# Optimization experiments

Measured on AMD Instinct MI355X. Metric: run time of the kernel, lower is better.

## Reference

```python
import jax, jax.numpy as jnp
import numpy as np

N, E = 50000, 800000
IN_DIM, HIDDEN, HEADS, EDGE_DIM, OUT_DIM = 128, 64, 4, 16, 1
NEG_SLOPE = 0.2


def gat_conv(x, src, dst, edge_attr, W, We, att_src, att_dst, att_edge, bias, heads, out_ch, concat):
    n = x.shape[0]
    h = (x @ W).reshape(n, heads, out_ch)                     # [N,H,C]
    a_src = jnp.einsum('nhc,hc->nh', h, att_src)              # [N,H]
    a_dst = jnp.einsum('nhc,hc->nh', h, att_dst)
    e = (edge_attr @ We).reshape(-1, heads, out_ch)           # [E,H,C]
    a_e = jnp.einsum('ehc,hc->eh', e, att_edge)               # [E,H]
    alpha = jax.nn.leaky_relu(a_src[src] + a_dst[dst] + a_e, NEG_SLOPE)  # [E,H]
    # per-destination-node softmax
    amax = jax.ops.segment_max(alpha, dst, num_segments=n)
    ex = jnp.exp(alpha - amax[dst])
    denom = jax.ops.segment_sum(ex, dst, num_segments=n)
    alpha = ex / (denom[dst] + 1e-16)
    msg = h[src] * alpha[..., None]                           # [E,H,C]
    out = jax.ops.segment_sum(msg, dst, num_segments=n)       # [N,H,C]
    out = out.reshape(n, heads * out_ch) if concat else out.mean(axis=1)
    return out + bias


def setup_inputs() -> dict:
    key = jax.random.key(0)
    ks = jax.random.split(key, 16)
    s = 0.1
    inp = {
        'x': jax.random.normal(ks[0], (N, IN_DIM), jnp.float32),
        'edge_index': jax.random.randint(ks[1], (2, E), 0, N, jnp.int32),
        'edge_attr': jax.random.normal(ks[2], (E, EDGE_DIM), jnp.float32),
        # layer 1: heads=4, concat=True
        'W1': jax.random.normal(ks[3], (IN_DIM, HEADS * HIDDEN), jnp.float32) * s,
        'We1': jax.random.normal(ks[4], (EDGE_DIM, HEADS * HIDDEN), jnp.float32) * s,
        'as1': jax.random.normal(ks[5], (HEADS, HIDDEN), jnp.float32) * s,
        'ad1': jax.random.normal(ks[6], (HEADS, HIDDEN), jnp.float32) * s,
        'ae1': jax.random.normal(ks[7], (HEADS, HIDDEN), jnp.float32) * s,
        'b1': jnp.zeros((HEADS * HIDDEN,), jnp.float32),
        # layer 2: heads=1, concat=False
        'W2': jax.random.normal(ks[8], (HEADS * HIDDEN, HIDDEN), jnp.float32) * s,
        'We2': jax.random.normal(ks[9], (EDGE_DIM, HIDDEN), jnp.float32) * s,
        'as2': jax.random.normal(ks[10], (1, HIDDEN), jnp.float32) * s,
        'ad2': jax.random.normal(ks[11], (1, HIDDEN), jnp.float32) * s,
        'ae2': jax.random.normal(ks[12], (1, HIDDEN), jnp.float32) * s,
        'b2': jnp.zeros((HIDDEN,), jnp.float32),
        'Wlin': jax.random.normal(ks[13], (HIDDEN, OUT_DIM), jnp.float32) * s,
        'blin': jnp.zeros((OUT_DIM,), jnp.float32),
    }
    return inp


def reference(x, edge_index, edge_attr, W1, We1, as1, ad1, ae1, b1, W2, We2, as2, ad2, ae2, b2, Wlin, blin):
    src, dst = edge_index[0], edge_index[1]
    h = jax.nn.relu(gat_conv(x, src, dst, edge_attr, W1, We1, as1, ad1, ae1, b1, HEADS, HIDDEN, True))
    h = jax.nn.relu(gat_conv(h, src, dst, edge_attr, W2, We2, as2, ad2, ae2, b2, 1, HIDDEN, False))
    return h @ Wlin + blin
```

## Files before the change

### kernel.cpp

```cpp
#include <hip/hip_runtime.h>
#include <math.h>

#define IN_DIM 128
#define HID 64
#define HEADS 4
#define EDGE_DIM 16
#define L1_OUT 256
#define NEG_SLOPE 0.2f
#define PAD 64

typedef __attribute__((ext_vector_type(8))) _Float16 half8_t;
typedef __attribute__((ext_vector_type(4))) _Float16 half4_t;
typedef __attribute__((ext_vector_type(4))) float floatx4;

__global__ __launch_bounds__(256) void prep_kernel(
    const float* __restrict__ W1, const float* __restrict__ as1, const float* __restrict__ ad1,
    const float* __restrict__ W2, const float* __restrict__ as2, const float* __restrict__ ad2,
    const float* __restrict__ We1, const float* __restrict__ ae1,
    const float* __restrict__ We2, const float* __restrict__ ae2,
    _Float16* __restrict__ W1t, _Float16* __restrict__ W2t,
    float* __restrict__ q1, float* __restrict__ q2,
    int* __restrict__ deg, int Nn) {
    int id = blockIdx.x * 256 + threadIdx.x;
    if (id < Nn) deg[id] = 0;
    if (id < 272 * 128) {
        int n = id >> 7, k = id & 127;
        float v = 0.f;
        if (n < 256) v = W1[k * 256 + n];
        else if (n < 260) { int h = n - 256; float s = 0.f;
            for (int c = 0; c < 64; ++c) s += W1[k * 256 + h * 64 + c] * as1[h * 64 + c]; v = s; }
        else if (n < 264) { int h = n - 260; float s = 0.f;
            for (int c = 0; c < 64; ++c) s += W1[k * 256 + h * 64 + c] * ad1[h * 64 + c]; v = s; }
        W1t[id] = (_Float16)v;
        return;
    }
    id -= 272 * 128;
    if (id < 80 * 256) {
        int n = id >> 8, k = id & 255;
        float v = 0.f;
        if (n < 64) v = W2[k * 64 + n];
        else if (n == 64) { float s = 0.f; for (int c = 0; c < 64; ++c) s += W2[k * 64 + c] * as2[c]; v = s; }
        else if (n == 65) { float s = 0.f; for (int c = 0; c < 64; ++c) s += W2[k * 64 + c] * ad2[c]; v = s; }
        W2t[id] = (_Float16)v;
        return;
    }
    id -= 80 * 256;
    if (id < 64) {
        int k = id >> 2, h = id & 3;
        float s = 0.f;
        for (int c = 0; c < 64; ++c) s += We1[k * 256 + h * 64 + c] * ae1[h * 64 + c];
        q1[id] = s;
        return;
    }
    id -= 64;
    if (id < 16) {
        float s = 0.f;
        for (int c = 0; c < 64; ++c) s += We2[id * 64 + c] * ae2[c];
        q2[id] = s;
    }
}

__global__ __launch_bounds__(256) void scatter_edge_kernel(
    const int* __restrict__ src, const int* __restrict__ dst,
    const float* __restrict__ ea, const float* __restrict__ q1,
    const float* __restrict__ q2, const float* __restrict__ asrc1,
    const float* __restrict__ adst1, int* __restrict__ deg,
    float4* __restrict__ rec, int E) {
    __shared__ float q[80];
    if (threadIdx.x < 64) q[threadIdx.x] = q1[threadIdx.x];
    else if (threadIdx.x < 80) q[threadIdx.x] = q2[threadIdx.x - 64];
    __syncthreads();
    int e = blockIdx.x * 256 + threadIdx.x;
    if (e >= E) return;
    const float4* p = (const float4*)(ea + (size_t)e * EDGE_DIM);
    float4 v0 = p[0], v1 = p[1], v2 = p[2], v3 = p[3];
    int sn = src[e];
    int d = dst[e];
    float4 as4 = *(const float4*)(asrc1 + (size_t)sn * 4);
    float4 ad4 = *(const float4*)(adst1 + (size_t)d * 4);
    float a[16] = {v0.x, v0.y, v0.z, v0.w, v1.x, v1.y, v1.z, v1.w,
                   v2.x, v2.y, v2.z, v2.w, v3.x, v3.y, v3.z, v3.w};
    float aeq[4];
#pragma unroll
    for (int h = 0; h < 4; ++h) {
        float s = 0.f;
#pragma unroll
        for (int k = 0; k < 16; ++k) s += a[k] * q[k * 4 + h];
        aeq[h] = s;
    }
    float r2 = 0.f;
#pragma unroll
    for (int k = 0; k < 16; ++k) r2 += a[k] * q[64 + k];
    const float* asp = (const float*)&as4;
    const float* adp = (const float*)&ad4;
    float4 hi;
    float* hp = (float*)&hi;
#pragma unroll
    for (int h = 0; h < 4; ++h) {
        float t = aeq[h] + asp[h] + adp[h];
        hp[h] = __expf(t > 0.f ? t : NEG_SLOPE * t);
    }
    int rank = atomicAdd(&deg[d], 1);
    if (rank >= PAD) return;
    size_t pos = (size_t)d * PAD + rank;
    float4 lo;
    lo.x = __int_as_float(sn); lo.y = r2; lo.z = 0.f; lo.w = 0.f;
    rec[pos * 2] = lo;
    rec[pos * 2 + 1] = hi;
}

template <int NTOT, int NFEAT, int HATT, bool A32>
__global__ __launch_bounds__(256) void gemm_att_kernel(
    const void* __restrict__ Av, const _Float16* __restrict__ Bt,
    _Float16* __restrict__ C, float* __restrict__ asrc, float* __restrict__ adst,
    int M, int K) {
    __shared__ _Float16 As[64][72];
    __shared__ _Float16 Bts[NTOT * 16][72];
    const int tid = threadIdx.x;
    const int lane = tid & 63;
    const int w = tid >> 6;
    const int row0 = blockIdx.x * 64;
    const int m = lane & 15;
    const int quad = lane >> 4;

    floatx4 acc[NTOT];
#pragma unroll
    for (int t = 0; t < NTOT; ++t) acc[t] = (floatx4){0.f, 0.f, 0.f, 0.f};

    const int ar = tid >> 2;
    const int ac = (tid & 3) * 16;

    for (int k0 = 0; k0 < K; k0 += 64) {
        half8_t a0 = {}, a1 = {};
        if (row0 + ar < M) {
            if constexpr (A32) {
                const float* A = (const float*)Av + (size_t)(row0 + ar) * K + k0 + ac;
                const float4* f = (const float4*)A;
                float4 f0 = f[0], f1 = f[1], f2 = f[2], f3 = f[3];
                a0 = (half8_t){(_Float16)f0.x, (_Float16)f0.y, (_Float16)f0.z, (_Float16)f0.w,
                               (_Float16)f1.x, (_Float16)f1.y, (_Float16)f1.z, (_Float16)f1.w};
                a1 = (half8_t){(_Float16)f2.x, (_Float16)f2.y, (_Float16)f2.z, (_Float16)f2.w,
                               (_Float16)f3.x, (_Float16)f3.y, (_Float16)f3.z, (_Float16)f3.w};
            } else {
                const half8_t* g = (const half8_t*)((const _Float16*)Av + (size_t)(row0 + ar) * K + k0 + ac);
                a0 = g[0]; a1 = g[1];
            }
        }
        *(half8_t*)&As[ar][ac] = a0;
        *(half8_t*)&As[ar][ac + 8] = a1;
        for (int idx = tid; idx < NTOT * 128; idx += 256) {
            int n = idx >> 3, j = (idx & 7) * 8;
            *(half8_t*)&Bts[n][j] = *(const half8_t*)(Bt + (size_t)n * K + k0 + j);
        }
        __syncthreads();
#pragma unroll
        for (int kc = 0; kc < 2; ++kc) {
            half8_t af = *(const half8_t*)&As[w * 16 + m][kc * 32 + quad * 8];
#pragma unroll
            for (int t = 0; t < NTOT; ++t) {
                half8_t bf = *(const half8_t*)&Bts[t * 16 + m][kc * 32 + quad * 8];
                acc[t] = __builtin_amdgcn_mfma_f32_16x16x32_f16(af, bf, acc[t], 0, 0, 0);
            }
        }
        __syncthreads();
    }
    const int TE = NFEAT / 16;
#pragma unroll
    for (int r = 0; r < 4; ++r) {
        int row = row0 + w * 16 + quad * 4 + r;
        if (row >= M) continue;
#pragma unroll
        for (int t = 0; t < TE; ++t)
            C[(size_t)row * NFEAT + t * 16 + m] = (_Float16)acc[t][r];
        float v = acc[TE][r];
        if (m < HATT) asrc[row * HATT + m] = v;
        else if (m < 2 * HATT) adst[row * HATT + (m - HATT)] = v;
    }
}

__global__ __launch_bounds__(256) void node1_kernel(
    const int* __restrict__ deg, const float4* __restrict__ rec,
    const _Float16* __restrict__ h1, const float* __restrict__ b1,
    _Float16* __restrict__ hr1, int Nn) {
    int lane = threadIdx.x & 63, wv = threadIdx.x >> 6;
    int n = blockIdx.x * 4 + wv;
    if (n >= Nn) return;
    int dg = __builtin_amdgcn_readfirstlane(deg[n]);
    if (dg > PAD) dg = PAD;
    size_t s0 = (size_t)n * PAD, s1 = s0 + dg;
    const int hh = lane >> 4;
    const int* reci = (const int*)rec;
    const float* recf = (const float*)rec;

    float ax = 0.f, ay = 0.f, az = 0.f, aw = 0.f, l = 0.f;
    size_t s = s0;
    for (; s + 3 < s1; s += 4) {
        int i0 = reci[(s) * 8];
        int i1 = reci[(s + 1) * 8];
        int i2 = reci[(s + 2) * 8];
        int i3 = reci[(s + 3) * 8];
        float e0 = recf[(s) * 8 + 4 + hh];
        float e1 = recf[(s + 1) * 8 + 4 + hh];
        float e2 = recf[(s + 2) * 8 + 4 + hh];
        float e3 = recf[(s + 3) * 8 + 4 + hh];
        half4_t v0 = *(const half4_t*)(h1 + (size_t)i0 * L1_OUT + lane * 4);
        half4_t v1 = *(const half4_t*)(h1 + (size_t)i1 * L1_OUT + lane * 4);
        half4_t v2 = *(const half4_t*)(h1 + (size_t)i2 * L1_OUT + lane * 4);
        half4_t v3 = *(const half4_t*)(h1 + (size_t)i3 * L1_OUT + lane * 4);
        l += (e0 + e1) + (e2 + e3);
        ax += e0 * (float)v0.x + e1 * (float)v1.x + e2 * (float)v2.x + e3 * (float)v3.x;
        ay += e0 * (float)v0.y + e1 * (float)v1.y + e2 * (float)v2.y + e3 * (float)v3.y;
        az += e0 * (float)v0.z + e1 * (float)v1.z + e2 * (float)v2.z + e3 * (float)v3.z;
        aw += e0 * (float)v0.w + e1 * (float)v1.w + e2 * (float)v2.w + e3 * (float)v3.w;
    }
    for (; s < s1; ++s) {
        int i0 = reci[s * 8];
        float e0 = recf[s * 8 + 4 + hh];
        half4_t v0 = *(const half4_t*)(h1 + (size_t)i0 * L1_OUT + lane * 4);
        l += e0;
        ax += e0 * (float)v0.x; ay += e0 * (float)v0.y;
        az += e0 * (float)v0.z; aw += e0 * (float)v0.w;
    }
    float inv = 1.f / (l + 1e-16f);
    float4 bb = *(const float4*)(b1 + lane * 4);
    half4_t out;
    out.x = (_Float16)fmaxf(ax * inv + bb.x, 0.f);
    out.y = (_Float16)fmaxf(ay * inv + bb.y, 0.f);
    out.z = (_Float16)fmaxf(az * inv + bb.z, 0.f);
    out.w = (_Float16)fmaxf(aw * inv + bb.w, 0.f);
    *(half4_t*)(hr1 + (size_t)n * L1_OUT + lane * 4) = out;
}

__global__ __launch_bounds__(256) void node2_kernel(
    const int* __restrict__ deg, const float4* __restrict__ rec,
    const float* __restrict__ asrc2, const float* __restrict__ adst2,
    const _Float16* __restrict__ h2, const float* __restrict__ b2,
    const float* __restrict__ Wlin, const float* __restrict__ blin,
    float* __restrict__ out, int Nn) {
    int lane = threadIdx.x & 63, wv = threadIdx.x >> 6;
    int n = blockIdx.x * 4 + wv;
    if (n >= Nn) return;
    int dg = __builtin_amdgcn_readfirstlane(deg[n]);
    if (dg > PAD) dg = PAD;
    size_t s0 = (size_t)n * PAD, s1 = s0 + dg;
    float adn = adst2[n];
    const int* reci = (const int*)rec;
    const float* recf = (const float*)rec;

    float l = 0.f, acc = 0.f;
    size_t s = s0;
    for (; s + 3 < s1; s += 4) {
        int n0 = reci[(s) * 8],     n1 = reci[(s + 1) * 8];
        int n2 = reci[(s + 2) * 8], n3 = reci[(s + 3) * 8];
        float q0 = recf[(s) * 8 + 1],     q1v = recf[(s + 1) * 8 + 1];
        float q2v = recf[(s + 2) * 8 + 1], q3 = recf[(s + 3) * 8 + 1];
        float t0 = q0 + asrc2[n0] + adn;
        float t1 = q1v + asrc2[n1] + adn;
        float t2 = q2v + asrc2[n2] + adn;
        float t3 = q3 + asrc2[n3] + adn;
        float v0 = (float)h2[(size_t)n0 * HID + lane];
        float v1 = (float)h2[(size_t)n1 * HID + lane];
        float v2 = (float)h2[(size_t)n2 * HID + lane];
        float v3 = (float)h2[(size_t)n3 * HID + lane];
        float e0 = __expf(t0 > 0.f ? t0 : NEG_SLOPE * t0);
        float e1 = __expf(t1 > 0.f ? t1 : NEG_SLOPE * t1);
        float e2 = __expf(t2 > 0.f ? t2 : NEG_SLOPE * t2);
        float e3 = __expf(t3 > 0.f ? t3 : NEG_SLOPE * t3);
        l += (e0 + e1) + (e2 + e3);
        acc += e0 * v0 + e1 * v1 + e2 * v2 + e3 * v3;
    }
    for (; s < s1; ++s) {
        int n0 = reci[s * 8];
        float q0 = recf[s * 8 + 1];
        float t0 = q0 + asrc2[n0] + adn;
        float e0 = __expf(t0 > 0.f ? t0 : NEG_SLOPE * t0);
        float v0 = (float)h2[(size_t)n0 * HID + lane];
        l += e0;
        acc += e0 * v0;
    }
    float res = fmaxf(acc / (l + 1e-16f) + b2[lane], 0.f);
    float t = res * Wlin[lane];
    for (int o = 32; o > 0; o >>= 1) t += __shfl_down(t, o);
    if (lane == 0) out[n] = t + blin[0];
}

extern "C" void kernel_launch(void* const* d_in, const int* in_sizes, int n_in,
                              void* d_out, int out_size, void* d_ws, size_t ws_size,
                              hipStream_t stream) {
    const float* x    = (const float*)d_in[0];
    const int*   ei   = (const int*)d_in[1];
    const float* ea   = (const float*)d_in[2];
    const float* W1   = (const float*)d_in[3];
    const float* We1  = (const float*)d_in[4];
    const float* as1  = (const float*)d_in[5];
    const float* ad1  = (const float*)d_in[6];
    const float* ae1  = (const float*)d_in[7];
    const float* b1   = (const float*)d_in[8];
    const float* W2   = (const float*)d_in[9];
    const float* We2  = (const float*)d_in[10];
    const float* as2  = (const float*)d_in[11];
    const float* ad2  = (const float*)d_in[12];
    const float* ae2  = (const float*)d_in[13];
    const float* b2   = (const float*)d_in[14];
    const float* Wlin = (const float*)d_in[15];
    const float* blin = (const float*)d_in[16];

    const int N = in_sizes[0] / IN_DIM;
    const int E = in_sizes[1] / 2;
    const int* src = ei;
    const int* dst = ei + E;

    char* base = (char*)d_ws;
    size_t off = 0;
    auto alloc = [&](size_t bytes) -> char* {
        char* p = base + off;
        off = (off + bytes + 255) & ~(size_t)255;
        return p;
    };
    int*      deg     = (int*)alloc((size_t)N * 4);
    float*    q1      = (float*)alloc(64 * 4);
    float*    q2      = (float*)alloc(16 * 4);
    _Float16* W1t     = (_Float16*)alloc((size_t)272 * 128 * 2);
    _Float16* W2t     = (_Float16*)alloc((size_t)80 * 256 * 2);
    float4*   rec     = (float4*)alloc((size_t)N * PAD * 32);
    float*    asrc1   = (float*)alloc((size_t)N * 4 * 4);
    float*    adst1   = (float*)alloc((size_t)N * 4 * 4);
    _Float16* h1      = (_Float16*)alloc((size_t)N * L1_OUT * 2);
    _Float16* hr1     = (_Float16*)alloc((size_t)N * L1_OUT * 2);
    _Float16* h2      = (_Float16*)alloc((size_t)N * HID * 2);
    float*    asrc2   = (float*)alloc((size_t)N * 4);
    float*    adst2   = (float*)alloc((size_t)N * 4);
    (void)ws_size; (void)n_in; (void)out_size;

    prep_kernel<<<218, 256, 0, stream>>>(W1, as1, ad1, W2, as2, ad2,
                                         We1, ae1, We2, ae2, W1t, W2t, q1, q2, deg, N);

    int mbl = (N + 63) / 64;
    gemm_att_kernel<17, 256, 4, true><<<mbl, 256, 0, stream>>>(x, W1t, h1, asrc1, adst1,
                                                               N, IN_DIM);
    scatter_edge_kernel<<<(E + 255) / 256, 256, 0, stream>>>(src, dst, ea, q1, q2,
                                                             asrc1, adst1, deg, rec, E);
    node1_kernel<<<(N + 3) / 4, 256, 0, stream>>>(deg, rec, h1, b1, hr1, N);
    gemm_att_kernel<5, 64, 1, false><<<mbl, 256, 0, stream>>>(hr1, W2t, h2, asrc2, adst2,
                                                              N, L1_OUT);
    node2_kernel<<<(N + 3) / 4, 256, 0, stream>>>(deg, rec, asrc2, adst2, h2, b2,
                                                  Wlin, blin, (float*)d_out, N);
}
```

Measured before the change: 330.2 us.

## Compact edge records to 16 bytes with fp16 weights, process 4 edges per thread

Each edge record shrinks from 32 to 16 bytes by storing the four layer-1 exp attention weights as fp16 next to the source index and the layer-2 edge term. This halves the record traffic written by the scatter kernel and read by both node kernels. The scatter kernel now handles four edges per thread, issuing the gathers and atomics for all four before the per-edge math so more memory operations are in flight. In exchange, the layer-1 weights lose precision, and exp values above the fp16 range could overflow.

```diff
diff --git a/kernel.cpp b/kernel.cpp
--- a/kernel.cpp
+++ b/kernel.cpp
@@ -12,6 +12,12 @@
 typedef __attribute__((ext_vector_type(8))) _Float16 half8_t;
 typedef __attribute__((ext_vector_type(4))) _Float16 half4_t;
 typedef __attribute__((ext_vector_type(4))) float floatx4;
+
+struct __align__(16) Rec16 {
+    int src;
+    float aeq2;
+    _Float16 e1[4];
+};
 
 __global__ __launch_bounds__(256) void prep_kernel(
     const float* __restrict__ W1, const float* __restrict__ as1, const float* __restrict__ ad1,
@@ -65,48 +71,73 @@
     const float* __restrict__ ea, const float* __restrict__ q1,
     const float* __restrict__ q2, const float* __restrict__ asrc1,
     const float* __restrict__ adst1, int* __restrict__ deg,
-    float4* __restrict__ rec, int E) {
+    float4* __restrict__ rec, int E, int T) {
     __shared__ float q[80];
     if (threadIdx.x < 64) q[threadIdx.x] = q1[threadIdx.x];
     else if (threadIdx.x < 80) q[threadIdx.x] = q2[threadIdx.x - 64];
     __syncthreads();
-    int e = blockIdx.x * 256 + threadIdx.x;
-    if (e >= E) return;
-    const float4* p = (const float4*)(ea + (size_t)e * EDGE_DIM);
-    float4 v0 = p[0], v1 = p[1], v2 = p[2], v3 = p[3];
-    int sn = src[e];
-    int d = dst[e];
-    float4 as4 = *(const float4*)(asrc1 + (size_t)sn * 4);
-    float4 ad4 = *(const float4*)(adst1 + (size_t)d * 4);
-    float a[16] = {v0.x, v0.y, v0.z, v0.w, v1.x, v1.y, v1.z, v1.w,
-                   v2.x, v2.y, v2.z, v2.w, v3.x, v3.y, v3.z, v3.w};
-    float aeq[4];
-#pragma unroll
-    for (int h = 0; h < 4; ++h) {
-        float s = 0.f;
-#pragma unroll
-        for (int k = 0; k < 16; ++k) s += a[k] * q[k * 4 + h];
-        aeq[h] = s;
-    }
-    float r2 = 0.f;
-#pragma unroll
-    for (int k = 0; k < 16; ++k) r2 += a[k] * q[64 + k];
-    const float* asp = (const float*)&as4;
-    const float* adp = (const float*)&ad4;
-    float4 hi;
-    float* hp = (float*)&hi;
-#pragma unroll
-    for (int h = 0; h < 4; ++h) {
-        float t = aeq[h] + asp[h] + adp[h];
-        hp[h] = __expf(t > 0.f ? t : NEG_SLOPE * t);
-    }
-    int rank = atomicAdd(&deg[d], 1);
-    if (rank >= PAD) return;
-    size_t pos = (size_t)d * PAD + rank;
-    float4 lo;
-    lo.x = __int_as_float(sn); lo.y = r2; lo.z = 0.f; lo.w = 0.f;
-    rec[pos * 2] = lo;
-    rec[pos * 2 + 1] = hi;
+    int t = blockIdx.x * 256 + threadIdx.x;
+
+#pragma unroll
+    for (int i = 0; i < 4; ++i) {
+        int e[1];
+        (void)e;
+    }
+    int e0 = t, e1i = t + T, e2i = t + 2 * T, e3i = t + 3 * T;
+    bool m0 = e0 < E, m1 = e1i < E, m2 = e2i < E, m3 = e3i < E;
+
+    int sn0 = m0 ? src[e0] : 0, sn1 = m1 ? src[e1i] : 0;
+    int sn2 = m2 ? src[e2i] : 0, sn3 = m3 ? src[e3i] : 0;
+    int d0 = m0 ? dst[e0] : 0, d1 = m1 ? dst[e1i] : 0;
+    int d2 = m2 ? dst[e2i] : 0, d3 = m3 ? dst[e3i] : 0;
+
+    float4 as0 = m0 ? *(const float4*)(asrc1 + (size_t)sn0 * 4) : make_float4(0, 0, 0, 0);
+    float4 as1v = m1 ? *(const float4*)(asrc1 + (size_t)sn1 * 4) : make_float4(0, 0, 0, 0);
+    float4 as2v = m2 ? *(const float4*)(asrc1 + (size_t)sn2 * 4) : make_float4(0, 0, 0, 0);
+    float4 as3 = m3 ? *(const float4*)(asrc1 + (size_t)sn3 * 4) : make_float4(0, 0, 0, 0);
+    float4 ad0 = m0 ? *(const float4*)(adst1 + (size_t)d0 * 4) : make_float4(0, 0, 0, 0);
+    float4 ad1v = m1 ? *(const float4*)(adst1 + (size_t)d1 * 4) : make_float4(0, 0, 0, 0);
+    float4 ad2v = m2 ? *(const float4*)(adst1 + (size_t)d2 * 4) : make_float4(0, 0, 0, 0);
+    float4 ad3 = m3 ? *(const float4*)(adst1 + (size_t)d3 * 4) : make_float4(0, 0, 0, 0);
+
+    int r0 = m0 ? atomicAdd(&deg[d0], 1) : PAD;
+    int r1 = m1 ? atomicAdd(&deg[d1], 1) : PAD;
+    int r2 = m2 ? atomicAdd(&deg[d2], 1) : PAD;
+    int r3 = m3 ? atomicAdd(&deg[d3], 1) : PAD;
+
+#pragma unroll
+    for (int i = 0; i < 4; ++i) {
+        int e = (i == 0) ? e0 : (i == 1) ? e1i : (i == 2) ? e2i : e3i;
+        bool m = (i == 0) ? m0 : (i == 1) ? m1 : (i == 2) ? m2 : m3;
+        if (!m) continue;
+        int rank = (i == 0) ? r0 : (i == 1) ? r1 : (i == 2) ? r2 : r3;
+        if (rank >= PAD) continue;
+        int d = (i == 0) ? d0 : (i == 1) ? d1 : (i == 2) ? d2 : d3;
+        int sn = (i == 0) ? sn0 : (i == 1) ? sn1 : (i == 2) ? sn2 : sn3;
+        float4 asv = (i == 0) ? as0 : (i == 1) ? as1v : (i == 2) ? as2v : as3;
+        float4 adv = (i == 0) ? ad0 : (i == 1) ? ad1v : (i == 2) ? ad2v : ad3;
+        const float4* p = (const float4*)(ea + (size_t)e * EDGE_DIM);
+        float4 v0 = p[0], v1 = p[1], v2 = p[2], v3 = p[3];
+        float a[16] = {v0.x, v0.y, v0.z, v0.w, v1.x, v1.y, v1.z, v1.w,
+                       v2.x, v2.y, v2.z, v2.w, v3.x, v3.y, v3.z, v3.w};
+        const float* asp = (const float*)&asv;
+        const float* adp = (const float*)&adv;
+        Rec16 rc;
+        rc.src = sn;
+        float r2s = 0.f;
+#pragma unroll
+        for (int k = 0; k < 16; ++k) r2s += a[k] * q[64 + k];
+        rc.aeq2 = r2s;
+#pragma unroll
+        for (int h = 0; h < 4; ++h) {
+            float s = 0.f;
+#pragma unroll
+            for (int k = 0; k < 16; ++k) s += a[k] * q[k * 4 + h];
+            float tv = s + asp[h] + adp[h];
+            rc.e1[h] = (_Float16)__expf(tv > 0.f ? tv : NEG_SLOPE * tv);
+        }
+        rec[(size_t)d * PAD + rank] = *(const float4*)&rc;
+    }
 }
 
 template <int NTOT, int NFEAT, int HATT, bool A32>
@@ -190,19 +221,19 @@
     size_t s0 = (size_t)n * PAD, s1 = s0 + dg;
     const int hh = lane >> 4;
     const int* reci = (const int*)rec;
-    const float* recf = (const float*)rec;
+    const _Float16* rech = (const _Float16*)rec;
 
     float ax = 0.f, ay = 0.f, az = 0.f, aw = 0.f, l = 0.f;
     size_t s = s0;
     for (; s + 3 < s1; s += 4) {
-        int i0 = reci[(s) * 8];
-        int i1 = reci[(s + 1) * 8];
-        int i2 = reci[(s + 2) * 8];
-        int i3 = reci[(s + 3) * 8];
-        float e0 = recf[(s) * 8 + 4 + hh];
-        float e1 = recf[(s + 1) * 8 + 4 + hh];
-        float e2 = recf[(s + 2) * 8 + 4 + hh];
-        float e3 = recf[(s + 3) * 8 + 4 + hh];
+        int i0 = reci[(s) * 4];
+        int i1 = reci[(s + 1) * 4];
+        int i2 = reci[(s + 2) * 4];
+        int i3 = reci[(s + 3) * 4];
+        float e0 = (float)rech[(s) * 8 + 4 + hh];
+        float e1 = (float)rech[(s + 1) * 8 + 4 + hh];
+        float e2 = (float)rech[(s + 2) * 8 + 4 + hh];
+        float e3 = (float)rech[(s + 3) * 8 + 4 + hh];
         half4_t v0 = *(const half4_t*)(h1 + (size_t)i0 * L1_OUT + lane * 4);
         half4_t v1 = *(const half4_t*)(h1 + (size_t)i1 * L1_OUT + lane * 4);
         half4_t v2 = *(const half4_t*)(h1 + (size_t)i2 * L1_OUT + lane * 4);
@@ -214,8 +245,8 @@
         aw += e0 * (float)v0.w + e1 * (float)v1.w + e2 * (float)v2.w + e3 * (float)v3.w;
     }
     for (; s < s1; ++s) {
-        int i0 = reci[s * 8];
-        float e0 = recf[s * 8 + 4 + hh];
+        int i0 = reci[s * 4];
+        float e0 = (float)rech[s * 8 + 4 + hh];
         half4_t v0 = *(const half4_t*)(h1 + (size_t)i0 * L1_OUT + lane * 4);
         l += e0;
         ax += e0 * (float)v0.x; ay += e0 * (float)v0.y;
@@ -250,10 +281,10 @@
     float l = 0.f, acc = 0.f;
     size_t s = s0;
     for (; s + 3 < s1; s += 4) {
-        int n0 = reci[(s) * 8],     n1 = reci[(s + 1) * 8];
-        int n2 = reci[(s + 2) * 8], n3 = reci[(s + 3) * 8];
-        float q0 = recf[(s) * 8 + 1],     q1v = recf[(s + 1) * 8 + 1];
-        float q2v = recf[(s + 2) * 8 + 1], q3 = recf[(s + 3) * 8 + 1];
+        int n0 = reci[(s) * 4],     n1 = reci[(s + 1) * 4];
+        int n2 = reci[(s + 2) * 4], n3 = reci[(s + 3) * 4];
+        float q0 = recf[(s) * 4 + 1],      q1v = recf[(s + 1) * 4 + 1];
+        float q2v = recf[(s + 2) * 4 + 1], q3 = recf[(s + 3) * 4 + 1];
         float t0 = q0 + asrc2[n0] + adn;
         float t1 = q1v + asrc2[n1] + adn;
         float t2 = q2v + asrc2[n2] + adn;
@@ -270,8 +301,8 @@
         acc += e0 * v0 + e1 * v1 + e2 * v2 + e3 * v3;
     }
     for (; s < s1; ++s) {
-        int n0 = reci[s * 8];
-        float q0 = recf[s * 8 + 1];
+        int n0 = reci[s * 4];
+        float q0 = recf[s * 4 + 1];
         float t0 = q0 + asrc2[n0] + adn;
         float e0 = __expf(t0 > 0.f ? t0 : NEG_SLOPE * t0);
         float v0 = (float)h2[(size_t)n0 * HID + lane];
@@ -322,7 +353,7 @@
     float*    q2      = (float*)alloc(16 * 4);
     _Float16* W1t     = (_Float16*)alloc((size_t)272 * 128 * 2);
     _Float16* W2t     = (_Float16*)alloc((size_t)80 * 256 * 2);
-    float4*   rec     = (float4*)alloc((size_t)N * PAD * 32);
+    float4*   rec     = (float4*)alloc((size_t)N * PAD * 16);
     float*    asrc1   = (float*)alloc((size_t)N * 4 * 4);
     float*    adst1   = (float*)alloc((size_t)N * 4 * 4);
     _Float16* h1      = (_Float16*)alloc((size_t)N * L1_OUT * 2);
@@ -338,8 +369,10 @@
     int mbl = (N + 63) / 64;
     gemm_att_kernel<17, 256, 4, true><<<mbl, 256, 0, stream>>>(x, W1t, h1, asrc1, adst1,
                                                                N, IN_DIM);
-    scatter_edge_kernel<<<(E + 255) / 256, 256, 0, stream>>>(src, dst, ea, q1, q2,
-                                                             asrc1, adst1, deg, rec, E);
+    int T = (E + 3) / 4;
+    int sbl = (T + 255) / 256;
+    scatter_edge_kernel<<<sbl, 256, 0, stream>>>(src, dst, ea, q1, q2,
+                                                 asrc1, adst1, deg, rec, E, sbl * 256);
     node1_kernel<<<(N + 3) / 4, 256, 0, stream>>>(deg, rec, h1, b1, hr1, N);
     gemm_att_kernel<5, 64, 1, false><<<mbl, 256, 0, stream>>>(hr1, W2t, h2, asrc2, adst2,
                                                               N, L1_OUT);
```

New measurement: 330.1 us. Within noise of the previous version (-0.0%).

## Pack edge records into 16 bytes with fp16 weights and unroll gathers by 8

Applied to the files above, without the earlier changes.

Shrinks each per-edge record from 32 to 16 bytes by storing the four layer-1 exp weights as fp16 alongside the source index and layer-2 edge term. Edge attribute loads and record stores use nontemporal hints. The node aggregation loops are unrolled to 8 with all loads issued before the math, giving more memory-level parallelism. Intent is to halve record write and read traffic and hide gather latency, at the cost of fp16 precision on the unnormalized attention weights, which could overflow for large logits.

```diff
diff --git a/kernel.cpp b/kernel.cpp
--- a/kernel.cpp
+++ b/kernel.cpp
@@ -12,6 +12,12 @@
 typedef __attribute__((ext_vector_type(8))) _Float16 half8_t;
 typedef __attribute__((ext_vector_type(4))) _Float16 half4_t;
 typedef __attribute__((ext_vector_type(4))) float floatx4;
+
+struct __align__(16) Rec16 {
+    int src;
+    float aeq2;
+    _Float16 e1[4];
+};
 
 __global__ __launch_bounds__(256) void prep_kernel(
     const float* __restrict__ W1, const float* __restrict__ as1, const float* __restrict__ ad1,
@@ -65,48 +71,43 @@
     const float* __restrict__ ea, const float* __restrict__ q1,
     const float* __restrict__ q2, const float* __restrict__ asrc1,
     const float* __restrict__ adst1, int* __restrict__ deg,
-    float4* __restrict__ rec, int E) {
+    floatx4* __restrict__ rec, int E) {
     __shared__ float q[80];
     if (threadIdx.x < 64) q[threadIdx.x] = q1[threadIdx.x];
     else if (threadIdx.x < 80) q[threadIdx.x] = q2[threadIdx.x - 64];
     __syncthreads();
     int e = blockIdx.x * 256 + threadIdx.x;
     if (e >= E) return;
-    const float4* p = (const float4*)(ea + (size_t)e * EDGE_DIM);
-    float4 v0 = p[0], v1 = p[1], v2 = p[2], v3 = p[3];
+    const floatx4* p = (const floatx4*)(ea + (size_t)e * EDGE_DIM);
+    floatx4 v0 = __builtin_nontemporal_load(p);
+    floatx4 v1 = __builtin_nontemporal_load(p + 1);
+    floatx4 v2 = __builtin_nontemporal_load(p + 2);
+    floatx4 v3 = __builtin_nontemporal_load(p + 3);
     int sn = src[e];
     int d = dst[e];
     float4 as4 = *(const float4*)(asrc1 + (size_t)sn * 4);
     float4 ad4 = *(const float4*)(adst1 + (size_t)d * 4);
     float a[16] = {v0.x, v0.y, v0.z, v0.w, v1.x, v1.y, v1.z, v1.w,
                    v2.x, v2.y, v2.z, v2.w, v3.x, v3.y, v3.z, v3.w};
-    float aeq[4];
+    Rec16 rc;
+    rc.src = sn;
+    float r2s = 0.f;
+#pragma unroll
+    for (int k = 0; k < 16; ++k) r2s += a[k] * q[64 + k];
+    rc.aeq2 = r2s;
+    const float* asp = (const float*)&as4;
+    const float* adp = (const float*)&ad4;
 #pragma unroll
     for (int h = 0; h < 4; ++h) {
         float s = 0.f;
 #pragma unroll
         for (int k = 0; k < 16; ++k) s += a[k] * q[k * 4 + h];
-        aeq[h] = s;
-    }
-    float r2 = 0.f;
-#pragma unroll
-    for (int k = 0; k < 16; ++k) r2 += a[k] * q[64 + k];
-    const float* asp = (const float*)&as4;
-    const float* adp = (const float*)&ad4;
-    float4 hi;
-    float* hp = (float*)&hi;
-#pragma unroll
-    for (int h = 0; h < 4; ++h) {
-        float t = aeq[h] + asp[h] + adp[h];
-        hp[h] = __expf(t > 0.f ? t : NEG_SLOPE * t);
+        float tv = s + asp[h] + adp[h];
+        rc.e1[h] = (_Float16)__expf(tv > 0.f ? tv : NEG_SLOPE * tv);
     }
     int rank = atomicAdd(&deg[d], 1);
     if (rank >= PAD) return;
-    size_t pos = (size_t)d * PAD + rank;
-    float4 lo;
-    lo.x = __int_as_float(sn); lo.y = r2; lo.z = 0.f; lo.w = 0.f;
-    rec[pos * 2] = lo;
-    rec[pos * 2 + 1] = hi;
+    __builtin_nontemporal_store(*(const floatx4*)&rc, rec + (size_t)d * PAD + rank);
 }
 
 template <int NTOT, int NFEAT, int HATT, bool A32>
@@ -179,7 +180,7 @@
 }
 
 __global__ __launch_bounds__(256) void node1_kernel(
-    const int* __restrict__ deg, const float4* __restrict__ rec,
+    const int* __restrict__ deg, const floatx4* __restrict__ rec,
     const _Float16* __restrict__ h1, const float* __restrict__ b1,
     _Float16* __restrict__ hr1, int Nn) {
     int lane = threadIdx.x & 63, wv = threadIdx.x >> 6;
@@ -190,32 +191,33 @@
     size_t s0 = (size_t)n * PAD, s1 = s0 + dg;
     const int hh = lane >> 4;
     const int* reci = (const int*)rec;
-    const float* recf = (const float*)rec;
+    const _Float16* rech = (const _Float16*)rec;
 
     float ax = 0.f, ay = 0.f, az = 0.f, aw = 0.f, l = 0.f;
     size_t s = s0;
-    for (; s + 3 < s1; s += 4) {
-        int i0 = reci[(s) * 8];
-        int i1 = reci[(s + 1) * 8];
-        int i2 = reci[(s + 2) * 8];
-        int i3 = reci[(s + 3) * 8];
-        float e0 = recf[(s) * 8 + 4 + hh];
-        float e1 = recf[(s + 1) * 8 + 4 + hh];
-        float e2 = recf[(s + 2) * 8 + 4 + hh];
-        float e3 = recf[(s + 3) * 8 + 4 + hh];
-        half4_t v0 = *(const half4_t*)(h1 + (size_t)i0 * L1_OUT + lane * 4);
-        half4_t v1 = *(const half4_t*)(h1 + (size_t)i1 * L1_OUT + lane * 4);
-        half4_t v2 = *(const half4_t*)(h1 + (size_t)i2 * L1_OUT + lane * 4);
-        half4_t v3 = *(const half4_t*)(h1 + (size_t)i3 * L1_OUT + lane * 4);
-        l += (e0 + e1) + (e2 + e3);
-        ax += e0 * (float)v0.x + e1 * (float)v1.x + e2 * (float)v2.x + e3 * (float)v3.x;
-        ay += e0 * (float)v0.y + e1 * (float)v1.y + e2 * (float)v2.y + e3 * (float)v3.y;
-        az += e0 * (float)v0.z + e1 * (float)v1.z + e2 * (float)v2.z + e3 * (float)v3.z;
-        aw += e0 * (float)v0.w + e1 * (float)v1.w + e2 * (float)v2.w + e3 * (float)v3.w;
+    for (; s + 7 < s1; s += 8) {
+        int idx[8];
+        float ew[8];
+        half4_t v[8];
+#pragma unroll
+        for (int j = 0; j < 8; ++j) idx[j] = reci[(s + j) * 4];
+#pragma unroll
+        for (int j = 0; j < 8; ++j) ew[j] = (float)rech[(s + j) * 8 + 4 + hh];
+#pragma unroll
+        for (int j = 0; j < 8; ++j)
+            v[j] = *(const half4_t*)(h1 + (size_t)idx[j] * L1_OUT + lane * 4);
+#pragma unroll
+        for (int j = 0; j < 8; ++j) {
+            l += ew[j];
+            ax += ew[j] * (float)v[j].x;
+            ay += ew[j] * (float)v[j].y;
+            az += ew[j] * (float)v[j].z;
+            aw += ew[j] * (float)v[j].w;
+        }
     }
     for (; s < s1; ++s) {
-        int i0 = reci[s * 8];
-        float e0 = recf[s * 8 + 4 + hh];
+        int i0 = reci[s * 4];
+        float e0 = (float)rech[s * 8 + 4 + hh];
         half4_t v0 = *(const half4_t*)(h1 + (size_t)i0 * L1_OUT + lane * 4);
         l += e0;
         ax += e0 * (float)v0.x; ay += e0 * (float)v0.y;
@@ -232,7 +234,7 @@
 }
 
 __global__ __launch_bounds__(256) void node2_kernel(
-    const int* __restrict__ deg, const float4* __restrict__ rec,
+    const int* __restrict__ deg, const floatx4* __restrict__ rec,
     const float* __restrict__ asrc2, const float* __restrict__ adst2,
     const _Float16* __restrict__ h2, const float* __restrict__ b2,
     const float* __restrict__ Wlin, const float* __restrict__ blin,
@@ -249,30 +251,28 @@
 
     float l = 0.f, acc = 0.f;
     size_t s = s0;
-    for (; s + 3 < s1; s += 4) {
-        int n0 = reci[(s) * 8],     n1 = reci[(s + 1) * 8];
-        int n2 = reci[(s + 2) * 8], n3 = reci[(s + 3) * 8];
-        float q0 = recf[(s) * 8 + 1],     q1v = recf[(s + 1) * 8 + 1];
-        float q2v = recf[(s + 2) * 8 + 1], q3 = recf[(s + 3) * 8 + 1];
-        float t0 = q0 + asrc2[n0] + adn;
-        float t1 = q1v + asrc2[n1] + adn;
-        float t2 = q2v + asrc2[n2] + adn;
-        float t3 = q3 + asrc2[n3] + adn;
-        float v0 = (float)h2[(size_t)n0 * HID + lane];
-        float v1 = (float)h2[(size_t)n1 * HID + lane];
-        float v2 = (float)h2[(size_t)n2 * HID + lane];
-        float v3 = (float)h2[(size_t)n3 * HID + lane];
-        float e0 = __expf(t0 > 0.f ? t0 : NEG_SLOPE * t0);
-        float e1 = __expf(t1 > 0.f ? t1 : NEG_SLOPE * t1);
-        float e2 = __expf(t2 > 0.f ? t2 : NEG_SLOPE * t2);
-        float e3 = __expf(t3 > 0.f ? t3 : NEG_SLOPE * t3);
-        l += (e0 + e1) + (e2 + e3);
-        acc += e0 * v0 + e1 * v1 + e2 * v2 + e3 * v3;
+    for (; s + 7 < s1; s += 8) {
+        int idx[8];
+        float aq[8], asv[8], v[8];
+#pragma unroll
+        for (int j = 0; j < 8; ++j) idx[j] = reci[(s + j) * 4];
+#pragma unroll
+        for (int j = 0; j < 8; ++j) aq[j] = recf[(s + j) * 4 + 1];
+#pragma unroll
+        for (int j = 0; j < 8; ++j) asv[j] = asrc2[idx[j]];
+#pragma unroll
+        for (int j = 0; j < 8; ++j) v[j] = (float)h2[(size_t)idx[j] * HID + lane];
+#pragma unroll
+        for (int j = 0; j < 8; ++j) {
+            float t = aq[j] + asv[j] + adn;
+            float e = __expf(t > 0.f ? t : NEG_SLOPE * t);
+            l += e;
+            acc += e * v[j];
+        }
     }
     for (; s < s1; ++s) {
-        int n0 = reci[s * 8];
-        float q0 = recf[s * 8 + 1];
-        float t0 = q0 + asrc2[n0] + adn;
+        int n0 = reci[s * 4];
+        float t0 = recf[s * 4 + 1] + asrc2[n0] + adn;
         float e0 = __expf(t0 > 0.f ? t0 : NEG_SLOPE * t0);
         float v0 = (float)h2[(size_t)n0 * HID + lane];
         l += e0;
@@ -322,7 +322,7 @@
     float*    q2      = (float*)alloc(16 * 4);
     _Float16* W1t     = (_Float16*)alloc((size_t)272 * 128 * 2);
     _Float16* W2t     = (_Float16*)alloc((size_t)80 * 256 * 2);
-    float4*   rec     = (float4*)alloc((size_t)N * PAD * 32);
+    floatx4*  rec     = (floatx4*)alloc((size_t)N * PAD * 16);
     float*    asrc1   = (float*)alloc((size_t)N * 4 * 4);
     float*    adst1   = (float*)alloc((size_t)N * 4 * 4);
     _Float16* h1      = (_Float16*)alloc((size_t)N * L1_OUT * 2);
```

New measurement: 335.4 us. Within noise of the previous version (+1.6%).
